# Kernel tuning notes

Measured on AMD Instinct MI355X. Metric: run time of the kernel, lower is better.

The kernel has to match this reference:

```python
import jax, jax.numpy as jnp
import numpy as np

B, N, NT, C, CO = 8, 12288, 3072, 256, 512
H0, W0 = 128, 96

def _grid_idx(loc, h, w):
    # loc in [-1,1] -> nearest grid cell index (matches token2map's round/clamp)
    loc = jnp.clip(jax.lax.stop_gradient(loc), -1.0, 1.0)
    xi = jnp.clip(jnp.round(0.5 * (loc[..., 0] + 1.0) * w - 0.5).astype(jnp.int32), 0, w - 1)
    yi = jnp.clip(jnp.round(0.5 * (loc[..., 1] + 1.0) * h - 0.5).astype(jnp.int32), 0, h - 1)
    return xi + yi * w

def _bn(x, gamma, beta):
    # BatchNorm (training-mode batch stats) over (B, N) per channel; x: (B, N, C)
    mean = x.mean(axis=(0, 1))
    var = ((x - mean) ** 2).mean(axis=(0, 1))
    return (x - mean) * jax.lax.rsqrt(var + 1e-5) * gamma + beta

def _token2map(x, loc, idx_agg, h, w):
    b, n, c = x.shape
    n0 = idx_agg.shape[1]
    seg = (_grid_idx(loc, h, w) + jnp.arange(b)[:, None] * (h * w)).reshape(-1)
    x_pt = jnp.take_along_axis(x, idx_agg[..., None], axis=1).reshape(b * n0, c)
    summed = jax.ops.segment_sum(x_pt, seg, num_segments=b * h * w)
    count = jax.ops.segment_sum(jnp.ones((b * n0,), x.dtype), seg, num_segments=b * h * w)
    x_map = summed / (count + 1e-6)[:, None]
    return x_map.reshape(b, h, w, c).transpose(0, 3, 1, 2)  # (B, C, H, W)

def _map2token(fmap, nt, loc, idx_agg_t, agg_weight_t):
    b, c, h, w = fmap.shape
    n0 = idx_agg_t.shape[1]
    idx_hw = _grid_idx(loc, h, w)
    fflat = fmap.reshape(b, c, h * w).transpose(0, 2, 1)  # (B, HW, C)
    feat = jnp.take_along_axis(fflat, idx_hw[..., None], axis=1)  # (B, N0, C)
    wgt = agg_weight_t.reshape(b, n0)
    seg = (idx_agg_t + jnp.arange(b)[:, None] * nt).reshape(-1)
    num = jax.ops.segment_sum((feat * wgt[..., None]).reshape(b * n0, c), seg, num_segments=b * nt)
    den = jax.ops.segment_sum(wgt.reshape(-1), seg, num_segments=b * nt) + 1e-6
    return (num / den[:, None]).reshape(b, nt, c)

def _token_downup(x_s, idx_agg_s, nt, idx_agg_t, agg_weight_t):
    b, s, c = x_s.shape
    n0 = idx_agg_s.shape[1]
    x_pt = jnp.take_along_axis(x_s, idx_agg_s[..., None], axis=1)  # (B, N0, C)
    wgt = agg_weight_t.reshape(b, n0)
    seg = (idx_agg_t + jnp.arange(b)[:, None] * nt).reshape(-1)
    num = jax.ops.segment_sum((x_pt * wgt[..., None]).reshape(b * n0, c), seg, num_segments=b * nt)
    den = jax.ops.segment_sum(wgt.reshape(-1), seg, num_segments=b * nt) + 1e-6
    return (num / den[:, None]).reshape(b, nt, c)

def setup_inputs():
    key = jax.random.key(0)
    ks = jax.random.split(key, 10)
    return {
        "x": jax.random.normal(ks[0], (B, N, C), jnp.float32),
        "loc_orig": jax.random.uniform(ks[1], (B, N, 2), jnp.float32, -1.0, 1.0),
        "idx_agg": jax.random.randint(ks[2], (B, N), 0, N),
        "agg_weight": jax.random.uniform(ks[3], (B, N, 1), jnp.float32),
        "x_t": jax.random.normal(ks[4], (B, NT, C), jnp.float32),
        "idx_agg_t": jax.random.randint(ks[5], (B, N), 0, NT),
        "agg_weight_t": jax.random.uniform(ks[6], (B, N, 1), jnp.float32),
        "H": H0, "W": W0,
        "dw_conv_w": jax.random.normal(ks[7], (C, 1, 3, 3), jnp.float32) * 0.1,
        "dw_skip_w": jax.random.normal(ks[8], (C, 1, 1, 1), jnp.float32) * 0.1,
        "norm1_gamma": jnp.ones((C,), jnp.float32),
        "norm1_beta": jnp.zeros((C,), jnp.float32),
        "conv_w": jax.random.normal(ks[9], (CO, C), jnp.float32) * (1.0 / np.sqrt(C)),
        "norm2_gamma": jnp.ones((CO,), jnp.float32),
        "norm2_beta": jnp.zeros((CO,), jnp.float32),
    }

def reference(x, loc_orig, idx_agg, agg_weight, x_t, idx_agg_t, agg_weight_t, H, W,
              dw_conv_w, dw_skip_w, norm1_gamma, norm1_beta, conv_w, norm2_gamma, norm2_beta):
    nt = x_t.shape[1]
    # token2map -> depthwise 3x3 stride-2 conv -> map2token (onto downsampled grid)
    x_map = _token2map(x, loc_orig, idx_agg, H, W)
    x_map = jax.lax.conv_general_dilated(
        x_map, dw_conv_w, window_strides=(2, 2), padding=((1, 1), (1, 1)),
        feature_group_count=x_map.shape[1],
        dimension_numbers=("NCHW", "OIHW", "NCHW"))
    x_map = _map2token(x_map, nt, loc_orig, idx_agg_t, agg_weight_t)
    # skip path: token_downup + 1x1 depthwise (per-channel scale)
    xd = _token_downup(x, idx_agg, nt, idx_agg_t, agg_weight_t)
    xd = xd * dw_skip_w.reshape(1, 1, -1)
    xd = xd + x_map
    xd = _bn(xd, norm1_gamma, norm1_beta)
    xd = jnp.einsum("bnc,oc->bno", xd, conv_w)  # 1x1 conv C -> CO
    xd = _bn(xd, norm2_gamma, norm2_beta)
    return jax.nn.relu(xd)
```

## Files before the change

kernel.cpp:

```cpp
#include <hip/hip_runtime.h>
#include <hip/hip_bf16.h>

using bf16 = __hip_bfloat16;
typedef __attribute__((ext_vector_type(8))) short bf16x8;
typedef __attribute__((ext_vector_type(4))) float f32x4;

#define BB   8
#define NN   12288
#define NTOK (BB*NN)
#define NTK  3072
#define CC   256
#define CCO  512
#define HH   128
#define WWI  96
#define HWIN (HH*WWI)
#define H2   64
#define W2   48
#define HW2  (H2*W2)
#define RR   (BB*NTK)

#define O_CONV  0LL
#define O_XD    6291456LL
#define O_AUX   9437184LL
#define O_ST2P  9437440LL
#define O_WT    12582912LL
#define O_ST1   12713984LL
#define O_ST2   12714496LL
#define O_AB1   12715520LL
#define O_B2    12716032LL
#define O_AB2   12716544LL
#define O_FLAG  12717568LL
#define O_META  12717572LL
#define O_OFF   12914180LL
#define O_LIST  13037060LL
#define O_L4    13233668LL

__device__ __forceinline__ float cvt(float v){ return v; }
__device__ __forceinline__ float cvt(bf16 v){ return __bfloat162float(v); }
template<typename T>
__device__ __forceinline__ float ld(const void* p, long long i){
    return cvt(((const T*)p)[i]);
}
__device__ __forceinline__ float bfu(unsigned short u){
    return __uint_as_float((unsigned)u << 16);
}
__device__ __forceinline__ unsigned short ubf(float f){
    bf16 h = __float2bfloat16(f);
    return *(unsigned short*)&h;
}
template<typename T>
__device__ __forceinline__ f32x4 ld4(const void* p, long long i);
template<>
__device__ __forceinline__ f32x4 ld4<bf16>(const void* p, long long i){
    const ushort4 u = *(const ushort4*)((const unsigned short*)p + i);
    return (f32x4){bfu(u.x), bfu(u.y), bfu(u.z), bfu(u.w)};
}
template<>
__device__ __forceinline__ f32x4 ld4<float>(const void* p, long long i){
    const float4 v = *(const float4*)((const float*)p + i);
    return (f32x4){v.x, v.y, v.z, v.w};
}

__global__ void k_flag(const float* __restrict__ locf, float* __restrict__ flag){
    if (threadIdx.x == 0){
        int bad = 0;
        for (int i = 0; i < 64; ++i){
            const float v = locf[i];
            if (!(v >= -1.0f && v <= 1.0f)) bad = 1;
        }
        flag[0] = bad ? 1.0f : 0.0f;
    }
}

__device__ __forceinline__ int2 gidx2(float lx, float ly, int h, int w){
    lx = fminf(fmaxf(lx, -1.f), 1.f);
    ly = fminf(fmaxf(ly, -1.f), 1.f);
    int xi = (int)rintf(0.5f*(lx+1.f)*(float)w - 0.5f);
    int yi = (int)rintf(0.5f*(ly+1.f)*(float)h - 0.5f);
    xi = min(max(xi,0), w-1); yi = min(max(yi,0), h-1);
    return make_int2(xi, yi);
}

template<typename T>
__device__ void meta_body(const void* loc, const int* __restrict__ iat,
                          int* __restrict__ off){
    const int tok = blockIdx.x*256 + threadIdx.x;
    const int b = tok / NN;
    const float lx = ld<T>(loc, 2LL*tok);
    const float ly = ld<T>(loc, 2LL*tok + 1);
    const int2 g1 = gidx2(lx, ly, HH, WWI);
    atomicAdd(&off[b*HWIN + g1.x + g1.y*WWI], 1);
    atomicAdd(&off[NTOK + b*NTK + iat[tok]], 1);
}
__global__ __launch_bounds__(256) void k_meta(
        const void* loc, const int* __restrict__ iat,
        const float* __restrict__ flag, int* __restrict__ off){
    if (flag[0] != 0.0f) meta_body<bf16>(loc, iat, off);
    else                 meta_body<float>(loc, iat, off);
}

#define SCN  (NTOK + RR)
#define SCB  120
__global__ __launch_bounds__(1024) void k_scan1(int* __restrict__ off, int* __restrict__ aux){
    __shared__ int sm[1024];
    const int tid = threadIdx.x;
    const int gid = blockIdx.x*1024 + tid;
    const int v = off[gid];
    sm[tid] = v;
    __syncthreads();
    for (int d = 1; d < 1024; d <<= 1){
        const int t = (tid >= d) ? sm[tid-d] : 0;
        __syncthreads();
        sm[tid] += t;
        __syncthreads();
    }
    off[gid] = sm[tid] - v;
    if (tid == 1023) aux[blockIdx.x] = sm[1023];
}
__global__ __launch_bounds__(128) void k_scan2(int* __restrict__ aux){
    __shared__ int sm[128];
    const int tid = threadIdx.x;
    const int v = (tid < SCB) ? aux[tid] : 0;
    sm[tid] = v;
    __syncthreads();
    for (int d = 1; d < 128; d <<= 1){
        const int t = (tid >= d) ? sm[tid-d] : 0;
        __syncthreads();
        sm[tid] += t;
        __syncthreads();
    }
    if (tid < SCB) aux[tid] = sm[tid] - v;
}
__global__ __launch_bounds__(1024) void k_scan3(int* __restrict__ off, const int* __restrict__ aux){
    off[blockIdx.x*1024 + threadIdx.x] += aux[blockIdx.x];
}

template<typename T>
__device__ void fill_body(const void* loc, const int* __restrict__ ia,
                          const int* __restrict__ iat, const void* wt,
                          int* __restrict__ off, int* __restrict__ list,
                          int4* __restrict__ list4){
    const int tok = blockIdx.x*256 + threadIdx.x;
    const int b = tok / NN;
    const float lx = ld<T>(loc, 2LL*tok);
    const float ly = ld<T>(loc, 2LL*tok + 1);
    const int2 g1 = gidx2(lx, ly, HH, WWI);
    const int2 g2 = gidx2(lx, ly, H2, W2);
    const float wv = ld<T>(wt, tok);
    const int rx = b*NN + ia[tok];
    const int pa = atomicAdd(&off[b*HWIN + g1.x + g1.y*WWI], 1);
    list[pa] = rx;
    const int pb = atomicAdd(&off[NTOK + b*NTK + iat[tok]], 1);
    int4 e; e.x = rx; e.y = b*HW2 + g2.x + g2.y*W2; e.z = __float_as_int(wv); e.w = 0;
    list4[pb] = e;
}
__global__ __launch_bounds__(256) void k_fill(
        const void* loc, const int* __restrict__ ia, const int* __restrict__ iat,
        const void* wt, const float* __restrict__ flag,
        int* __restrict__ off, int* __restrict__ list, int4* __restrict__ list4){
    if (flag[0] != 0.0f) fill_body<bf16>(loc, ia, iat, wt, off, list, list4);
    else                 fill_body<float>(loc, ia, iat, wt, off, list, list4);
}

#define PFC 4
template<typename T>
__device__ void conv_body(const void* x, const void* dww,
                          const int* __restrict__ off, const int* __restrict__ list,
                          bf16* __restrict__ conv){
    __shared__ f32x4 red[3][64];
    const int tid = threadIdx.x;
    const int kh = tid >> 6;
    const int lane = tid & 63;
    const int ch0 = lane*4;
    const int cell = blockIdx.x;
    const int b = cell / HW2;
    const int p = cell % HW2;
    const int oh = p / W2, ow = p % W2;
    const int ih = 2*oh - 1 + kh;
    f32x4 part = (f32x4){0.f,0.f,0.f,0.f};
    if (ih >= 0){
        const int gbase = b*HWIN + ih*WWI + 2*ow - 1;
        const int e0 = (gbase >= 0) ? off[gbase] : 0;
        const int e1 = off[gbase+1];
        const int e2 = off[gbase+2];
        const int ms = (ow > 0) ? off[gbase-1] : e0;
        f32x4 w0, w1, w2;
        #pragma unroll
        for (int c = 0; c < 4; ++c){
            w0[c] = ld<T>(dww, (long long)(ch0+c)*9 + kh*3 + 0);
            w1[c] = ld<T>(dww, (long long)(ch0+c)*9 + kh*3 + 1);
            w2[c] = ld<T>(dww, (long long)(ch0+c)*9 + kh*3 + 2);
        }
        f32x4 b0 = (f32x4){0.f,0.f,0.f,0.f};
        f32x4 b1 = (f32x4){0.f,0.f,0.f,0.f};
        f32x4 b2 = (f32x4){0.f,0.f,0.f,0.f};
        int idx = ms;
        while (idx < e2){
            int t[PFC];
            #pragma unroll
            for (int k = 0; k < PFC; ++k)
                t[k] = (idx + k < e2) ? list[idx + k] : 0;
            #pragma unroll
            for (int k = 0; k < PFC; ++k){
                if (idx + k < e2){
                    const f32x4 xv = ld4<T>(x, (long long)t[k]*CC + ch0);
                    const int gi = idx + k;
                    if (gi < e0)      b0 += xv;
                    else if (gi < e1) b1 += xv;
                    else              b2 += xv;
                }
            }
            idx += PFC;
        }
        const float r0 = 1.0f/((float)(e0 - ms) + 1e-6f);
        const float r1 = 1.0f/((float)(e1 - e0) + 1e-6f);
        const float r2 = 1.0f/((float)(e2 - e1) + 1e-6f);
        #pragma unroll
        for (int c = 0; c < 4; ++c)
            part[c] = w0[c]*b0[c]*r0 + w1[c]*b1[c]*r1 + w2[c]*b2[c]*r2;
    }
    red[kh][lane] = part;
    __syncthreads();
    if (kh == 0){
        const f32x4 t0 = red[0][lane];
        const f32x4 t1 = red[1][lane];
        const f32x4 t2 = red[2][lane];
        ushort4 o;
        o.x = ubf(t0[0]+t1[0]+t2[0]);
        o.y = ubf(t0[1]+t1[1]+t2[1]);
        o.z = ubf(t0[2]+t1[2]+t2[2]);
        o.w = ubf(t0[3]+t1[3]+t2[3]);
        *(ushort4*)((unsigned short*)conv + (long long)cell*CC + ch0) = o;
    }
}
__global__ __launch_bounds__(192) void k_conv(
        const void* x, const void* dww, const float* __restrict__ flag,
        const int* __restrict__ off, const int* __restrict__ list,
        bf16* __restrict__ conv){
    if (flag[0] != 0.0f) conv_body<bf16>(x, dww, off, list, conv);
    else                 conv_body<float>(x, dww, off, list, conv);
}

#define PFN 8
template<typename T>
__device__ void num_body(const void* x, const bf16* __restrict__ conv,
                         const void* skw,
                         const int* __restrict__ off, const int4* __restrict__ list4,
                         bf16* __restrict__ xdf){
    const int tid = threadIdx.x;
    const int wave = tid >> 6;
    const int lane = tid & 63;
    const int ch0 = lane*4;
    const f32x4 sk = ld4<T>(skw, ch0);
    const int gt = blockIdx.x*4 + wave;
    const int gj = NTOK + gt;
    int offv = 0;
    if (lane < 2) offv = off[gj - 1 + lane];
    const int s = __shfl(offv, 0);
    const int e = __shfl(offv, 1);
    f32x4 a = (f32x4){0.f,0.f,0.f,0.f};
    float den = 0.f;
    int idx = s;
    while (idx < e){
        int4 t[PFN];
        #pragma unroll
        for (int k = 0; k < PFN; ++k)
            if (idx + k < e) t[k] = list4[idx + k];
        #pragma unroll
        for (int k = 0; k < PFN; ++k){
            if (idx + k < e){
                const float wv = __int_as_float(t[k].z);
                const f32x4 xv = ld4<T>(x, (long long)t[k].x*CC + ch0);
                const f32x4 cv = ld4<bf16>(conv, (long long)t[k].y*CC + ch0);
                #pragma unroll
                for (int c = 0; c < 4; ++c)
                    a[c] += wv*(sk[c]*xv[c] + cv[c]);
                den += wv;
            }
        }
        idx += PFN;
    }
    const float rl = 1.0f/(den + 1e-6f);
    ushort4 o;
    o.x = ubf(a[0]*rl); o.y = ubf(a[1]*rl);
    o.z = ubf(a[2]*rl); o.w = ubf(a[3]*rl);
    const long long bi = (long long)(gt >> 4)*4096 + (long long)(ch0 >> 3)*128
                       + (long long)(gt & 15)*8 + (ch0 & 7);
    *(ushort4*)((unsigned short*)xdf + bi) = o;
}
__global__ __launch_bounds__(256) void k_num(
        const void* x, const bf16* __restrict__ conv, const void* skw,
        const int* __restrict__ off, const int4* __restrict__ list4,
        const float* __restrict__ flag,
        bf16* __restrict__ xdf){
    if (flag[0] != 0.0f) num_body<bf16>(x, conv, skw, off, list4, xdf);
    else                 num_body<float>(x, conv, skw, off, list4, xdf);
}

__global__ __launch_bounds__(512) void k_st1(const bf16* __restrict__ xdf,
                                             float* __restrict__ st1){
    __shared__ float ss[CC], sq[CC];
    const int tid = threadIdx.x;
    if (tid < CC){ ss[tid] = 0.f; sq[tid] = 0.f; }
    __syncthreads();
    const int tl = tid & 15;
    const int cg = tid >> 4;
    const int c0 = cg*8;
    float s[8], q[8];
    #pragma unroll
    for (int k = 0; k < 8; ++k){ s[k] = 0.f; q[k] = 0.f; }
    for (int sb = blockIdx.x; sb < RR/16; sb += gridDim.x){
        const long long o = (long long)sb*512 + cg*16 + tl;
        const bf16x8 v = *((const bf16x8*)xdf + o);
        #pragma unroll
        for (int k = 0; k < 8; ++k){
            const float f = bfu((unsigned short)v[k]);
            s[k] += f; q[k] += f*f;
        }
    }
    #pragma unroll
    for (int k = 0; k < 8; ++k){
        atomicAdd(&ss[c0+k], s[k]);
        atomicAdd(&sq[c0+k], q[k]);
    }
    __syncthreads();
    if (tid < CC){
        atomicAdd(&st1[tid], ss[tid]);
        atomicAdd(&st1[CC + tid], sq[tid]);
    }
}

template<typename T>
__device__ void bn1_body(const float* __restrict__ st1, const void* g1, const void* b1,
                         float* __restrict__ ab1){
    const int tid = threadIdx.x;
    const float mean = st1[tid]/(float)RR;
    const float var  = st1[CC + tid]/(float)RR - mean*mean;
    const float a  = ld<T>(g1, tid) * rsqrtf(var + 1e-5f);
    ab1[tid] = a;
    ab1[CC + tid] = ld<T>(b1, tid) - mean*a;
}
__global__ __launch_bounds__(256) void k_bn1(
        const float* __restrict__ st1, const void* g1, const void* b1,
        const float* __restrict__ flag, float* __restrict__ ab1){
    if (flag[0] != 0.0f) bn1_body<bf16>(st1, g1, b1, ab1);
    else                 bn1_body<float>(st1, g1, b1, ab1);
}

template<typename T>
__device__ void wt_body(const void* cw, const float* __restrict__ ab1,
                        bf16* __restrict__ wTf, float* __restrict__ bias2){
    const int c = blockIdx.x, o = threadIdx.x;
    const float w = ld<T>(cw, (long long)o*CC + c);
    wTf[(((long long)(o >> 4)*32 + (c >> 3))*16 + (o & 15))*8 + (c & 7)] =
        __float2bfloat16(w * ab1[c]);
    atomicAdd(&bias2[o], w * ab1[CC + c]);
}
__global__ __launch_bounds__(512) void k_wt(
        const void* cw, const float* __restrict__ ab1,
        const float* __restrict__ flag, bf16* __restrict__ wTf,
        float* __restrict__ bias2){
    if (flag[0] != 0.0f) wt_body<bf16>(cw, ab1, wTf, bias2);
    else                 wt_body<float>(cw, ab1, wTf, bias2);
}

__global__ __launch_bounds__(256) void k_gemm(
        const bf16* __restrict__ xdf, const bf16* __restrict__ wTf,
        const float* __restrict__ bias2, const float* __restrict__ flag,
        void* __restrict__ y, float* __restrict__ st2p){
    __shared__ float ss[128], sq[128];
    const int tid = threadIdx.x;
    if (tid < 128){ ss[tid] = 0.f; sq[tid] = 0.f; }
    __syncthreads();
    const int wave = tid >> 6;
    const int lane = tid & 63;
    const int l16 = lane & 15;
    const int lq  = lane >> 4;
    const int mb = blockIdx.x;
    const int nb = blockIdx.y;
    const int mt = mb*4 + wave;
    const int n0t = nb*8;
    const short* ap = (const short*)xdf + ((long long)mt*32 + lq)*128 + (long long)l16*8;
    const short* bp = (const short*)wTf + ((long long)n0t*32 + lq)*128 + (long long)l16*8;
    f32x4 acc[8];
    #pragma unroll
    for (int nt = 0; nt < 8; ++nt) acc[nt] = (f32x4){0.f,0.f,0.f,0.f};
    #pragma unroll
    for (int kg0 = 0; kg0 < 8; ++kg0){
        const bf16x8 af = *((const bf16x8*)(ap + kg0*512));
        #pragma unroll
        for (int nt = 0; nt < 8; ++nt){
            const bf16x8 bfr = *((const bf16x8*)(bp + (long long)nt*4096 + kg0*512));
            acc[nt] = __builtin_amdgcn_mfma_f32_16x16x32_bf16(af, bfr, acc[nt], 0, 0, 0);
        }
    }
    const int row0 = mt*16 + lq*4;
    const bool isbf = (flag[0] != 0.0f);
    #pragma unroll
    for (int nt = 0; nt < 8; ++nt){
        const int col = nb*128 + nt*16 + l16;
        const float bz = bias2[col];
        float s = 0.f, q = 0.f;
        float v[4];
        #pragma unroll
        for (int r = 0; r < 4; ++r){
            v[r] = acc[nt][r] + bz;
            s += v[r]; q += v[r]*v[r];
        }
        if (isbf){
            bf16* yo = (bf16*)y;
            #pragma unroll
            for (int r = 0; r < 4; ++r)
                yo[(long long)(row0 + r)*CCO + col] = __float2bfloat16(v[r]);
        } else {
            float* yo = (float*)y;
            #pragma unroll
            for (int r = 0; r < 4; ++r)
                yo[(long long)(row0 + r)*CCO + col] = v[r];
        }
        s += __shfl_xor(s, 16); s += __shfl_xor(s, 32);
        q += __shfl_xor(q, 16); q += __shfl_xor(q, 32);
        if (lq == 0){
            atomicAdd(&ss[nt*16 + l16], s);
            atomicAdd(&sq[nt*16 + l16], q);
        }
    }
    __syncthreads();
    if (tid < 128){
        const int slot = (mb & 7)*1024;
        atomicAdd(&st2p[slot + nb*128 + tid], ss[tid]);
        atomicAdd(&st2p[slot + 512 + nb*128 + tid], sq[tid]);
    }
}

template<typename T>
__device__ void bn2_body(const float* __restrict__ st2p, const void* g2, const void* b2,
                         float* __restrict__ ab2){
    const int tid = threadIdx.x;
    float s = 0.f, q = 0.f;
    #pragma unroll
    for (int p = 0; p < 8; ++p){
        s += st2p[p*1024 + tid];
        q += st2p[p*1024 + 512 + tid];
    }
    const float mean = s/(float)RR;
    const float var  = q/(float)RR - mean*mean;
    const float a = ld<T>(g2, tid) * rsqrtf(var + 1e-5f);
    ab2[tid] = a;
    ab2[CCO + tid] = ld<T>(b2, tid) - mean*a;
}
__global__ __launch_bounds__(512) void k_bn2(
        const float* __restrict__ st2p, const void* g2, const void* b2,
        const float* __restrict__ flag, float* __restrict__ ab2){
    if (flag[0] != 0.0f) bn2_body<bf16>(st2p, g2, b2, ab2);
    else                 bn2_body<float>(st2p, g2, b2, ab2);
}

__global__ __launch_bounds__(256) void k_out(
        void* __restrict__ y, const float* __restrict__ ab2,
        const float* __restrict__ flag){
    const long long i0 = ((long long)blockIdx.x*256 + threadIdx.x)*4;
    const int o0 = (int)(i0 & (CCO-1));
    if (flag[0] != 0.0f){
        unsigned short* p = (unsigned short*)y;
        ushort4 u = *(ushort4*)(p + i0);
        float v0 = bfu(u.x)*ab2[o0  ] + ab2[CCO + o0  ];
        float v1 = bfu(u.y)*ab2[o0+1] + ab2[CCO + o0+1];
        float v2 = bfu(u.z)*ab2[o0+2] + ab2[CCO + o0+2];
        float v3 = bfu(u.w)*ab2[o0+3] + ab2[CCO + o0+3];
        u.x = ubf(fmaxf(v0,0.f)); u.y = ubf(fmaxf(v1,0.f));
        u.z = ubf(fmaxf(v2,0.f)); u.w = ubf(fmaxf(v3,0.f));
        *(ushort4*)(p + i0) = u;
    } else {
        float* p = (float*)y;
        float4 v = *(float4*)(p + i0);
        v.x = fmaxf(v.x*ab2[o0  ] + ab2[CCO + o0  ], 0.f);
        v.y = fmaxf(v.y*ab2[o0+1] + ab2[CCO + o0+1], 0.f);
        v.z = fmaxf(v.z*ab2[o0+2] + ab2[CCO + o0+2], 0.f);
        v.w = fmaxf(v.w*ab2[o0+3] + ab2[CCO + o0+3], 0.f);
        *(float4*)(p + i0) = v;
    }
}

extern "C" void kernel_launch(void* const* d_in, const int* in_sizes, int n_in,
                              void* d_out, int out_size, void* d_ws, size_t ws_size,
                              hipStream_t stream){
    (void)in_sizes; (void)n_in; (void)out_size; (void)ws_size;
    const void* x   = d_in[0];
    const void* loc = d_in[1];
    const int*  ia  = (const int*)d_in[2];
    const int*  iat = (const int*)d_in[5];
    const void* wt  = d_in[6];
    const void* dww = d_in[9];
    const void* skw = d_in[10];
    const void* g1  = d_in[11];
    const void* b1  = d_in[12];
    const void* cw  = d_in[13];
    const void* g2  = d_in[14];
    const void* b2  = d_in[15];
    float* ws = (float*)d_ws;
    float* flag = ws + O_FLAG;
    int*  off  = (int*)(ws + O_OFF);
    int*  list = (int*)(ws + O_LIST);
    int4* list4 = (int4*)(ws + O_L4);
    int*  aux  = (int*)(ws + O_AUX);
    bf16* conv = (bf16*)(ws + O_CONV);
    bf16* xdf  = (bf16*)(ws + O_XD);
    bf16* wTf  = (bf16*)(ws + O_WT);

    hipMemsetAsync(ws + O_ST1, 0, (size_t)2560*4, stream);
    hipMemsetAsync(ws + O_ST2P, 0, (size_t)8192*4, stream);
    hipMemsetAsync(off, 0, (size_t)SCN*4, stream);

    k_flag<<<dim3(1), dim3(64), 0, stream>>>((const float*)loc, flag);

    k_meta<<<dim3(NTOK/256), dim3(256), 0, stream>>>(loc, iat, flag, off);

    k_scan1<<<dim3(SCB), dim3(1024), 0, stream>>>(off, aux);
    k_scan2<<<dim3(1), dim3(128), 0, stream>>>(aux);
    k_scan3<<<dim3(SCB), dim3(1024), 0, stream>>>(off, aux);

    k_fill<<<dim3(NTOK/256), dim3(256), 0, stream>>>(
        loc, ia, iat, wt, flag, off, list, list4);

    k_conv<<<dim3(BB*HW2), dim3(192), 0, stream>>>(x, dww, flag, off, list, conv);

    k_num<<<dim3(RR/4), dim3(256), 0, stream>>>(
        x, conv, skw, off, list4, flag, xdf);

    k_st1<<<dim3(192), dim3(512), 0, stream>>>(xdf, ws + O_ST1);

    k_bn1<<<dim3(1), dim3(256), 0, stream>>>(
        ws + O_ST1, g1, b1, flag, ws + O_AB1);

    k_wt<<<dim3(CC), dim3(512), 0, stream>>>(cw, ws + O_AB1, flag, wTf, ws + O_B2);

    k_gemm<<<dim3(384, 4), dim3(256), 0, stream>>>(
        xdf, wTf, ws + O_B2, flag, d_out, ws + O_ST2P);

    k_bn2<<<dim3(1), dim3(512), 0, stream>>>(ws + O_ST2P, g2, b2, flag, ws + O_AB2);

    k_out<<<dim3((RR*CCO)/1024, 1), dim3(256), 0, stream>>>(d_out, ws + O_AB2, flag);
}
```

Baseline: 363.3 us.

## Cut kernel launches by fusing init, scan, BN1 stats and weight prep

```diff
diff --git a/kernel.cpp b/kernel.cpp
--- a/kernel.cpp
+++ b/kernel.cpp
@@ -24,13 +24,12 @@
 #define O_AUX   9437184LL
 #define O_ST2P  9437440LL
 #define O_WT    12582912LL
-#define O_ST1   12713984LL
-#define O_ST2   12714496LL
+#define O_TK    12713984LL
 #define O_AB1   12715520LL
 #define O_B2    12716032LL
 #define O_AB2   12716544LL
 #define O_FLAG  12717568LL
-#define O_META  12717572LL
+#define O_S1P   12717572LL
 #define O_OFF   12914180LL
 #define O_LIST  13037060LL
 #define O_L4    13233668LL
@@ -61,14 +60,24 @@
     return (f32x4){v.x, v.y, v.z, v.w};
 }
 
-__global__ void k_flag(const float* __restrict__ locf, float* __restrict__ flag){
-    if (threadIdx.x == 0){
-        int bad = 0;
-        for (int i = 0; i < 64; ++i){
-            const float v = locf[i];
-            if (!(v >= -1.0f && v <= 1.0f)) bad = 1;
-        }
-        flag[0] = bad ? 1.0f : 0.0f;
+#define SCN  (NTOK + RR)
+#define SCB  120
+
+__global__ __launch_bounds__(256) void k_init(
+        const float* __restrict__ locf, int* __restrict__ off,
+        int* __restrict__ tickets, float* __restrict__ flag){
+    const int gid = blockIdx.x*256 + threadIdx.x;
+    off[gid] = 0;
+    if (blockIdx.x == 0){
+        if (threadIdx.x < 2) tickets[threadIdx.x] = 0;
+        if (threadIdx.x == 0){
+            int bad = 0;
+            for (int i = 0; i < 64; ++i){
+                const float v = locf[i];
+                if (!(v >= -1.0f && v <= 1.0f)) bad = 1;
+            }
+            flag[0] = bad ? 1.0f : 0.0f;
+        }
     }
 }
 
@@ -99,8 +108,6 @@
     else                 meta_body<float>(loc, iat, off);
 }
 
-#define SCN  (NTOK + RR)
-#define SCB  120
 __global__ __launch_bounds__(1024) void k_scan1(int* __restrict__ off, int* __restrict__ aux){
     __shared__ int sm[1024];
     const int tid = threadIdx.x;
@@ -117,22 +124,19 @@
     off[gid] = sm[tid] - v;
     if (tid == 1023) aux[blockIdx.x] = sm[1023];
 }
-__global__ __launch_bounds__(128) void k_scan2(int* __restrict__ aux){
-    __shared__ int sm[128];
-    const int tid = threadIdx.x;
-    const int v = (tid < SCB) ? aux[tid] : 0;
-    sm[tid] = v;
-    __syncthreads();
-    for (int d = 1; d < 128; d <<= 1){
-        const int t = (tid >= d) ? sm[tid-d] : 0;
-        __syncthreads();
-        sm[tid] += t;
-        __syncthreads();
-    }
-    if (tid < SCB) aux[tid] = sm[tid] - v;
-}
 __global__ __launch_bounds__(1024) void k_scan3(int* __restrict__ off, const int* __restrict__ aux){
-    off[blockIdx.x*1024 + threadIdx.x] += aux[blockIdx.x];
+    __shared__ int sm[SCB];
+    __shared__ int sRun;
+    const int tid = threadIdx.x;
+    if (tid < SCB) sm[tid] = aux[tid];
+    __syncthreads();
+    if (tid == 0){
+        int r = 0;
+        for (int j = 0; j < (int)blockIdx.x; ++j) r += sm[j];
+        sRun = r;
+    }
+    __syncthreads();
+    off[blockIdx.x*1024 + tid] += sRun;
 }
 
 template<typename T>
@@ -162,7 +166,6 @@
     else                 fill_body<float>(loc, ia, iat, wt, off, list, list4);
 }
 
-#define PFC 4
 template<typename T>
 __device__ void conv_body(const void* x, const void* dww,
                           const int* __restrict__ off, const int* __restrict__ list,
@@ -196,21 +199,33 @@
         f32x4 b2 = (f32x4){0.f,0.f,0.f,0.f};
         int idx = ms;
         while (idx < e2){
-            int t[PFC];
-            #pragma unroll
-            for (int k = 0; k < PFC; ++k)
-                t[k] = (idx + k < e2) ? list[idx + k] : 0;
-            #pragma unroll
-            for (int k = 0; k < PFC; ++k){
-                if (idx + k < e2){
-                    const f32x4 xv = ld4<T>(x, (long long)t[k]*CC + ch0);
-                    const int gi = idx + k;
-                    if (gi < e0)      b0 += xv;
-                    else if (gi < e1) b1 += xv;
-                    else              b2 += xv;
+            const int cnt = min(e2 - idx, 64);
+            const int tokv = (lane < cnt) ? list[idx + lane] : 0;
+            int j = 0;
+            for (; j + 4 <= cnt; j += 4){
+                int oxs[4];
+                #pragma unroll
+                for (int u = 0; u < 4; ++u)
+                    oxs[u] = __shfl(tokv, j+u)*CC + ch0;
+                f32x4 xv[4];
+                #pragma unroll
+                for (int u = 0; u < 4; ++u) xv[u] = ld4<T>(x, (long long)oxs[u]);
+                #pragma unroll
+                for (int u = 0; u < 4; ++u){
+                    const int gi = idx + j + u;
+                    if (gi < e0)      b0 += xv[u];
+                    else if (gi < e1) b1 += xv[u];
+                    else              b2 += xv[u];
                 }
             }
-            idx += PFC;
+            for (; j < cnt; ++j){
+                const f32x4 xv = ld4<T>(x, (long long)(__shfl(tokv, j)*CC + ch0));
+                const int gi = idx + j;
+                if (gi < e0)      b0 += xv;
+                else if (gi < e1) b1 += xv;
+                else              b2 += xv;
+            }
+            idx += cnt;
         }
         const float r0 = 1.0f/((float)(e0 - ms) + 1e-6f);
         const float r1 = 1.0f/((float)(e1 - e0) + 1e-6f);
@@ -297,9 +312,12 @@
     else                 num_body<float>(x, conv, skw, off, list4, xdf);
 }
 
-__global__ __launch_bounds__(512) void k_st1(const bf16* __restrict__ xdf,
-                                             float* __restrict__ st1){
+template<typename T>
+__device__ void st1_body(const bf16* __restrict__ xdf, float* __restrict__ s1p,
+                         int* __restrict__ ticket, const void* g1, const void* b1,
+                         float* __restrict__ ab1){
     __shared__ float ss[CC], sq[CC];
+    __shared__ int isLast;
     const int tid = threadIdx.x;
     if (tid < CC){ ss[tid] = 0.f; sq[tid] = 0.f; }
     __syncthreads();
@@ -325,43 +343,64 @@
     }
     __syncthreads();
     if (tid < CC){
-        atomicAdd(&st1[tid], ss[tid]);
-        atomicAdd(&st1[CC + tid], sq[tid]);
-    }
-}
-
-template<typename T>
-__device__ void bn1_body(const float* __restrict__ st1, const void* g1, const void* b1,
-                         float* __restrict__ ab1){
-    const int tid = threadIdx.x;
-    const float mean = st1[tid]/(float)RR;
-    const float var  = st1[CC + tid]/(float)RR - mean*mean;
-    const float a  = ld<T>(g1, tid) * rsqrtf(var + 1e-5f);
-    ab1[tid] = a;
-    ab1[CC + tid] = ld<T>(b1, tid) - mean*a;
-}
-__global__ __launch_bounds__(256) void k_bn1(
-        const float* __restrict__ st1, const void* g1, const void* b1,
+        s1p[blockIdx.x*512 + tid]       = ss[tid];
+        s1p[blockIdx.x*512 + 256 + tid] = sq[tid];
+    }
+    __syncthreads();
+    if (tid == 0){
+        __threadfence();
+        const int old = atomicAdd(ticket, 1);
+        isLast = (old == (int)gridDim.x - 1) ? 1 : 0;
+    }
+    __syncthreads();
+    if (isLast && tid < CC){
+        __threadfence();
+        float su = 0.f, qu = 0.f;
+        const volatile float* vp = s1p;
+        for (int bi = 0; bi < 192; ++bi){
+            su += vp[bi*512 + tid];
+            qu += vp[bi*512 + 256 + tid];
+        }
+        const float mean = su/(float)RR;
+        const float var  = qu/(float)RR - mean*mean;
+        const float a = ld<T>(g1, tid) * rsqrtf(var + 1e-5f);
+        ab1[tid] = a;
+        ab1[CC + tid] = ld<T>(b1, tid) - mean*a;
+    }
+}
+__global__ __launch_bounds__(512) void k_st1(
+        const bf16* __restrict__ xdf, float* __restrict__ s1p,
+        int* __restrict__ ticket, const void* g1, const void* b1,
         const float* __restrict__ flag, float* __restrict__ ab1){
-    if (flag[0] != 0.0f) bn1_body<bf16>(st1, g1, b1, ab1);
-    else                 bn1_body<float>(st1, g1, b1, ab1);
+    if (flag[0] != 0.0f) st1_body<bf16>(xdf, s1p, ticket, g1, b1, ab1);
+    else                 st1_body<float>(xdf, s1p, ticket, g1, b1, ab1);
 }
 
 template<typename T>
 __device__ void wt_body(const void* cw, const float* __restrict__ ab1,
-                        bf16* __restrict__ wTf, float* __restrict__ bias2){
-    const int c = blockIdx.x, o = threadIdx.x;
+                        bf16* __restrict__ wTf, float* __restrict__ bias2,
+                        float* __restrict__ st2p){
+    __shared__ float red[256];
+    const int o = blockIdx.x;
+    const int c = threadIdx.x;
+    if (o < 32) st2p[o*256 + c] = 0.f;
     const float w = ld<T>(cw, (long long)o*CC + c);
     wTf[(((long long)(o >> 4)*32 + (c >> 3))*16 + (o & 15))*8 + (c & 7)] =
         __float2bfloat16(w * ab1[c]);
-    atomicAdd(&bias2[o], w * ab1[CC + c]);
-}
-__global__ __launch_bounds__(512) void k_wt(
+    red[c] = w * ab1[CC + c];
+    __syncthreads();
+    for (int d = 128; d > 0; d >>= 1){
+        if (c < d) red[c] += red[c + d];
+        __syncthreads();
+    }
+    if (c == 0) bias2[o] = red[0];
+}
+__global__ __launch_bounds__(256) void k_wt(
         const void* cw, const float* __restrict__ ab1,
         const float* __restrict__ flag, bf16* __restrict__ wTf,
-        float* __restrict__ bias2){
-    if (flag[0] != 0.0f) wt_body<bf16>(cw, ab1, wTf, bias2);
-    else                 wt_body<float>(cw, ab1, wTf, bias2);
+        float* __restrict__ bias2, float* __restrict__ st2p){
+    if (flag[0] != 0.0f) wt_body<bf16>(cw, ab1, wTf, bias2, st2p);
+    else                 wt_body<float>(cw, ab1, wTf, bias2, st2p);
 }
 
 __global__ __launch_bounds__(256) void k_gemm(
@@ -504,20 +543,17 @@
     int*  list = (int*)(ws + O_LIST);
     int4* list4 = (int4*)(ws + O_L4);
     int*  aux  = (int*)(ws + O_AUX);
+    int*  tickets = (int*)(ws + O_TK);
     bf16* conv = (bf16*)(ws + O_CONV);
     bf16* xdf  = (bf16*)(ws + O_XD);
     bf16* wTf  = (bf16*)(ws + O_WT);
 
-    hipMemsetAsync(ws + O_ST1, 0, (size_t)2560*4, stream);
-    hipMemsetAsync(ws + O_ST2P, 0, (size_t)8192*4, stream);
-    hipMemsetAsync(off, 0, (size_t)SCN*4, stream);
-
-    k_flag<<<dim3(1), dim3(64), 0, stream>>>((const float*)loc, flag);
+    k_init<<<dim3(SCN/256), dim3(256), 0, stream>>>(
+        (const float*)loc, off, tickets, flag);
 
     k_meta<<<dim3(NTOK/256), dim3(256), 0, stream>>>(loc, iat, flag, off);
 
     k_scan1<<<dim3(SCB), dim3(1024), 0, stream>>>(off, aux);
-    k_scan2<<<dim3(1), dim3(128), 0, stream>>>(aux);
     k_scan3<<<dim3(SCB), dim3(1024), 0, stream>>>(off, aux);
 
     k_fill<<<dim3(NTOK/256), dim3(256), 0, stream>>>(
@@ -528,12 +564,11 @@
     k_num<<<dim3(RR/4), dim3(256), 0, stream>>>(
         x, conv, skw, off, list4, flag, xdf);
 
-    k_st1<<<dim3(192), dim3(512), 0, stream>>>(xdf, ws + O_ST1);
-
-    k_bn1<<<dim3(1), dim3(256), 0, stream>>>(
-        ws + O_ST1, g1, b1, flag, ws + O_AB1);
-
-    k_wt<<<dim3(CC), dim3(512), 0, stream>>>(cw, ws + O_AB1, flag, wTf, ws + O_B2);
+    k_st1<<<dim3(192), dim3(512), 0, stream>>>(
+        xdf, ws + O_S1P, &tickets[1], g1, b1, flag, ws + O_AB1);
+
+    k_wt<<<dim3(CCO), dim3(256), 0, stream>>>(
+        cw, ws + O_AB1, flag, wTf, ws + O_B2, ws + O_ST2P);
 
     k_gemm<<<dim3(384, 4), dim3(256), 0, stream>>>(
         xdf, wTf, ws + O_B2, flag, d_out, ws + O_ST2P);
```

New measurement: 424.6 us. 1.17x slower.
